# Performance work log

Measured on AMD Instinct MI355X. Metric: run time of the kernel, lower is better.

## Reference

```python
import jax, jax.numpy as jnp
import numpy as np

N = 100000        # points
C_IN = 64         # in_planes
C_OUT = 64        # out_planes (== mid_planes)
SHARE = 8         # share_planes
NS = 16           # nsample
CW = C_OUT // SHARE  # attention channels (8)
EPS = 1e-5


def _bn(x, gamma, beta):
    # PointBatchNorm in training mode: normalize over all axes except channel (last)
    ax = tuple(range(x.ndim - 1))
    m = jnp.mean(x, axis=ax)
    v = jnp.var(x, axis=ax)
    return gamma * (x - m) * jax.lax.rsqrt(v + EPS) + beta


def setup_inputs() -> dict:
    key = jax.random.key(0)
    ks = jax.random.split(key, 20)
    s = 0.05
    inp = {
        "p": jax.random.normal(ks[0], (N, 3), jnp.float32) * 5.0,
        "x": jax.random.normal(ks[1], (N, C_IN), jnp.float32),
        "o": jnp.array([N], jnp.int32),
        "idx": jax.random.randint(ks[2], (N, NS), 0, N, jnp.int32),
        # q/k/v linears
        "Wq": jax.random.normal(ks[3], (C_IN, C_OUT), jnp.float32) * s,
        "bq": jnp.zeros((C_OUT,), jnp.float32),
        "Wk": jax.random.normal(ks[4], (C_IN, C_OUT), jnp.float32) * s,
        "bk": jnp.zeros((C_OUT,), jnp.float32),
        "Wv": jax.random.normal(ks[5], (C_IN, C_OUT), jnp.float32) * s,
        "bv": jnp.zeros((C_OUT,), jnp.float32),
        # linear_p: Linear(3,3) -> BN(3) -> ReLU -> Linear(3,out)
        "Wp1": jax.random.normal(ks[6], (3, 3), jnp.float32) * 0.5,
        "bp1": jnp.zeros((3,), jnp.float32),
        "gp": jnp.ones((3,), jnp.float32),
        "betap": jnp.zeros((3,), jnp.float32),
        "Wp2": jax.random.normal(ks[7], (3, C_OUT), jnp.float32) * s,
        "bp2": jnp.zeros((C_OUT,), jnp.float32),
        # linear_w: BN(mid)->ReLU->Linear(mid, CW)->BN(CW)->ReLU->Linear(CW, CW)
        "gw1": jnp.ones((C_OUT,), jnp.float32),
        "bw1": jnp.zeros((C_OUT,), jnp.float32),
        "Ww1": jax.random.normal(ks[8], (C_OUT, CW), jnp.float32) * s,
        "bww1": jnp.zeros((CW,), jnp.float32),
        "gw2": jnp.ones((CW,), jnp.float32),
        "bw2": jnp.zeros((CW,), jnp.float32),
        "Ww2": jax.random.normal(ks[9], (CW, CW), jnp.float32) * s,
        "bww2": jnp.zeros((CW,), jnp.float32),
    }
    return inp


def reference(p, x, o, idx,
              Wq, bq, Wk, bk, Wv, bv,
              Wp1, bp1, gp, betap, Wp2, bp2,
              gw1, bw1, Ww1, bww1, gw2, bw2, Ww2, bww2):
    relu = jax.nn.relu
    x_q = x @ Wq + bq                       # [n, mid]
    x_k = x @ Wk + bk                       # [n, mid]
    x_v = x @ Wv + bv                       # [n, out]
    # knn_query_and_group: gather neighbors (idx precomputed), with relative xyz
    p_r0 = p[idx] - p[:, None, :]           # [n, ns, 3]
    xk_g = x_k[idx]                         # [n, ns, mid]
    xv_g = x_v[idx]                         # [n, ns, out]
    # linear_p
    p_r = relu(_bn(p_r0 @ Wp1 + bp1, gp, betap)) @ Wp2 + bp2   # [n, ns, out]
    # einops.reduce 'n ns (i j) -> n ns j' with j=mid_planes: i==1 -> identity
    r_qk = xk_g - x_q[:, None, :] + p_r     # [n, ns, mid]
    # linear_w
    w = relu(_bn(r_qk, gw1, bw1)) @ Ww1 + bww1          # [n, ns, CW]
    w = relu(_bn(w, gw2, bw2)) @ Ww2 + bww2             # [n, ns, CW]
    w = jax.nn.softmax(w, axis=1)                        # softmax over neighbors
    # shared-channel weighted sum
    v = (xv_g + p_r).reshape(N, NS, SHARE, CW)           # [n, ns, s, i]
    out = jnp.einsum('ntsi,nti->nsi', v, w)              # [n, s, i]
    return out.reshape(N, C_OUT)
```

## Files before the change

kernel.cpp:

```cpp
#include <hip/hip_runtime.h>
#include <math.h>

#define NPTS 100000
#define NSAMP 16
#define NROWS (NPTS*NSAMP)
#define EPS 1e-5f

#define NQKV ((NPTS + 63)/64)
#define GRID_B 1024
#define GRID_C 2048
#define GRID_D 2048
#define GRID_E 2048

#define S_BN1A 0
#define S_BN1B 4
#define S_BN2A 8
#define S_BN2B 72
#define S_BN3A 136
#define S_BN3B 144
#define S_PARTB 160
#define S_PARTC (S_PARTB + GRID_B*8)
#define S_PARTD (S_PARTC + GRID_C*128)

typedef __attribute__((ext_vector_type(8))) _Float16 f16x8;
typedef __attribute__((ext_vector_type(4))) float f32x4;

__device__ __forceinline__ float bf2f(unsigned short u) {
    return __uint_as_float(((unsigned int)u) << 16);
}
__device__ __forceinline__ unsigned int cvt_pk_bf16(float lo, float hi) {
    unsigned int r;
    asm("v_cvt_pk_bf16_f32 %0, %1, %2" : "=v"(r) : "v"(lo), "v"(hi));
    return r;
}
__device__ __forceinline__ float rlF(float v, int t) {
    return __int_as_float(__builtin_amdgcn_readlane(__float_as_int(v), t));
}

__global__ __launch_bounds__(256) void qkv_bn1_kernel(
    const float* __restrict__ x,
    const float* __restrict__ Wq, const float* __restrict__ bq,
    const float* __restrict__ Wk, const float* __restrict__ bk,
    const float* __restrict__ Wv, const float* __restrict__ bv,
    unsigned short* __restrict__ xqb, unsigned short* __restrict__ xkb,
    unsigned short* __restrict__ xvb,
    const float* __restrict__ p, const int* __restrict__ idx,
    const float* __restrict__ Wp1, const float* __restrict__ bp1,
    unsigned short* __restrict__ tb, float* __restrict__ part)
{
    __shared__ __align__(16) float xsh[64][68];
    __shared__ __align__(16) float wsh[64][64];
    __shared__ float red16[4][6];
    const int tid = threadIdx.x;

    if (blockIdx.x >= NQKV) {
        const int b = blockIdx.x - NQKV;
        float w9[9], bb[3];
        #pragma unroll
        for (int i = 0; i < 9; ++i) w9[i] = Wp1[i];
        #pragma unroll
        for (int i = 0; i < 3; ++i) bb[i] = bp1[i];

        float s0=0.f,s1=0.f,s2=0.f,q0=0.f,q1=0.f,q2=0.f;
        for (int row = b*256 + tid; row < NROWS; row += GRID_B*256) {
            const int n = row >> 4;
            const int j = idx[row];
            const float d0 = p[j*3+0] - p[n*3+0];
            const float d1 = p[j*3+1] - p[n*3+1];
            const float d2 = p[j*3+2] - p[n*3+2];
            const float t0 = d0*w9[0] + d1*w9[3] + d2*w9[6] + bb[0];
            const float t1 = d0*w9[1] + d1*w9[4] + d2*w9[7] + bb[1];
            const float t2 = d0*w9[2] + d1*w9[5] + d2*w9[8] + bb[2];
            uint2 o;
            o.x = cvt_pk_bf16(t0, t1);
            o.y = cvt_pk_bf16(t2, 0.f);
            *(uint2*)&tb[(size_t)row*4] = o;
            s0 += t0; s1 += t1; s2 += t2;
            q0 += t0*t0; q1 += t1*t1; q2 += t2*t2;
        }
        #pragma unroll
        for (int m = 32; m >= 1; m >>= 1) {
            s0 += __shfl_xor(s0, m); s1 += __shfl_xor(s1, m); s2 += __shfl_xor(s2, m);
            q0 += __shfl_xor(q0, m); q1 += __shfl_xor(q1, m); q2 += __shfl_xor(q2, m);
        }
        const int lane = tid & 63, wid = tid >> 6;
        if (lane == 0) {
            red16[wid][0]=s0; red16[wid][1]=s1; red16[wid][2]=s2;
            red16[wid][3]=q0; red16[wid][4]=q1; red16[wid][5]=q2;
        }
        __syncthreads();
        if (tid < 6)
            part[b*8 + tid] = red16[0][tid]+red16[1][tid]+red16[2][tid]+red16[3][tid];
        return;
    }

    const int r0 = blockIdx.x * 64;
    {
        const int row = tid >> 4, c4 = tid & 15;
        #pragma unroll
        for (int rr = 0; rr < 4; ++rr) {
            const int r = row + rr*16;
            const int gr = r0 + r;
            float4 v = (gr < NPTS) ? *(const float4*)&x[(size_t)gr*64 + c4*4]
                                   : make_float4(0.f, 0.f, 0.f, 0.f);
            *(float4*)&xsh[r][c4*4] = v;
        }
    }

    const int tr = tid >> 4, tc = tid & 15;

    for (int m = 0; m < 3; ++m) {
        const float* __restrict__ W  = (m == 0) ? Wq : (m == 1) ? Wk : Wv;
        const float* __restrict__ bs = (m == 0) ? bq : (m == 1) ? bk : bv;
        unsigned short* __restrict__ dst = (m == 0) ? xqb : (m == 1) ? xkb : xvb;

        __syncthreads();
        for (int l = tid; l < 1024; l += 256)
            *(float4*)&wsh[l >> 4][(l & 15)*4] = *(const float4*)&W[l*4];
        __syncthreads();

        float acc[4][4];
        {
            const float4 b4 = *(const float4*)&bs[tc*4];
            #pragma unroll
            for (int rr = 0; rr < 4; ++rr) {
                acc[rr][0] = b4.x; acc[rr][1] = b4.y;
                acc[rr][2] = b4.z; acc[rr][3] = b4.w;
            }
        }

        #pragma unroll 4
        for (int k4 = 0; k4 < 16; ++k4) {
            float4 xr[4];
            #pragma unroll
            for (int rr = 0; rr < 4; ++rr)
                xr[rr] = *(const float4*)&xsh[tr + 16*rr][k4*4];
            float4 wr[4];
            #pragma unroll
            for (int kk = 0; kk < 4; ++kk)
                wr[kk] = *(const float4*)&wsh[k4*4 + kk][tc*4];
            #pragma unroll
            for (int rr = 0; rr < 4; ++rr) {
                acc[rr][0] += xr[rr].x*wr[0].x + xr[rr].y*wr[1].x + xr[rr].z*wr[2].x + xr[rr].w*wr[3].x;
                acc[rr][1] += xr[rr].x*wr[0].y + xr[rr].y*wr[1].y + xr[rr].z*wr[2].y + xr[rr].w*wr[3].y;
                acc[rr][2] += xr[rr].x*wr[0].z + xr[rr].y*wr[1].z + xr[rr].z*wr[2].z + xr[rr].w*wr[3].z;
                acc[rr][3] += xr[rr].x*wr[0].w + xr[rr].y*wr[1].w + xr[rr].z*wr[2].w + xr[rr].w*wr[3].w;
            }
        }

        #pragma unroll
        for (int rr = 0; rr < 4; ++rr) {
            const int gr = r0 + tr + 16*rr;
            if (gr < NPTS) {
                uint2 o;
                o.x = cvt_pk_bf16(acc[rr][0], acc[rr][1]);
                o.y = cvt_pk_bf16(acc[rr][2], acc[rr][3]);
                *(uint2*)&dst[(size_t)gr*64 + tc*4] = o;
            }
        }
    }
}

__global__ __launch_bounds__(256) void bn_fin_kernel(
    const float* __restrict__ part, int nblk, int stride, int nch,
    const float* __restrict__ g, const float* __restrict__ beta,
    float* __restrict__ aout, float* __restrict__ bout)
{
    const int c = blockIdx.x;
    const int tid = threadIdx.x;
    float s = 0.f, q = 0.f;
    for (int b = tid; b < nblk; b += 256) {
        s += part[(size_t)b*stride + c];
        q += part[(size_t)b*stride + nch + c];
    }
    #pragma unroll
    for (int m = 32; m >= 1; m >>= 1) { s += __shfl_xor(s, m); q += __shfl_xor(q, m); }
    __shared__ float rs[4], rq[4];
    if ((tid & 63) == 0) { rs[tid >> 6] = s; rq[tid >> 6] = q; }
    __syncthreads();
    if (tid == 0) {
        s = rs[0]+rs[1]+rs[2]+rs[3];
        q = rq[0]+rq[1]+rq[2]+rq[3];
        const float inv = 1.0f / (float)NROWS;
        const float mean = s * inv;
        const float var = fmaxf(q * inv - mean*mean, 0.f);
        const float a = g[c] * rsqrtf(var + EPS);
        aout[c] = a;
        bout[c] = beta[c] - a * mean;
    }
}

__global__ __launch_bounds__(256, 8) void bn2_stats_kernel(
    const int* __restrict__ idx, const unsigned short* __restrict__ tb,
    const unsigned short* __restrict__ xqb, const unsigned short* __restrict__ xkb,
    const float* __restrict__ Wp2, const float* __restrict__ bp2,
    const float* __restrict__ st, float* __restrict__ part)
{
    const int tid = threadIdx.x, lane = tid & 63, wid = tid >> 6;
    float a1[3], b1[3];
    #pragma unroll
    for (int i = 0; i < 3; ++i) { a1[i] = st[S_BN1A+i]; b1[i] = st[S_BN1B+i]; }
    const float wc0 = Wp2[lane], wc1 = Wp2[64+lane], wc2 = Wp2[128+lane], bpc = bp2[lane];
    const int lane16 = lane & 15;

    float s = 0.f, q = 0.f;
    const int nw = gridDim.x * 4;
    for (int pt = blockIdx.x*4 + wid; pt < NPTS; pt += nw) {
        const float xqc = bf2f(xqb[(size_t)pt*64 + lane]);
        const int jreg = idx[pt*16 + lane16];
        const uint2 tv = *(const uint2*)&tb[(size_t)(pt*16 + lane16)*4];
        const float t0 = bf2f((unsigned short)tv.x);
        const float t1 = bf2f((unsigned short)(tv.x >> 16));
        const float t2 = bf2f((unsigned short)tv.y);
        const float h0 = fmaxf(a1[0]*t0 + b1[0], 0.f);
        const float h1 = fmaxf(a1[1]*t1 + b1[1], 0.f);
        const float h2 = fmaxf(a1[2]*t2 + b1[2], 0.f);

        #pragma unroll
        for (int t = 0; t < 16; ++t) {
            const int jt = __builtin_amdgcn_readlane(jreg, t);
            const float g0 = rlF(h0, t), g1 = rlF(h1, t), g2 = rlF(h2, t);
            const float pr = fmaf(g0, wc0, fmaf(g1, wc1, fmaf(g2, wc2, bpc)));
            const float r = bf2f(xkb[(size_t)jt*64 + lane]) - xqc + pr;
            s += r; q = fmaf(r, r, q);
        }
    }
    __shared__ float redS[4][64], redQ[4][64];
    redS[wid][lane] = s; redQ[wid][lane] = q;
    __syncthreads();
    if (tid < 64) {
        const float S = redS[0][tid]+redS[1][tid]+redS[2][tid]+redS[3][tid];
        const float Q = redQ[0][tid]+redQ[1][tid]+redQ[2][tid]+redQ[3][tid];
        part[(size_t)blockIdx.x*128 + tid] = S;
        part[(size_t)blockIdx.x*128 + 64 + tid] = Q;
    }
}

__global__ __launch_bounds__(256, 8) void w1_kernel(
    const int* __restrict__ idx, const unsigned short* __restrict__ tb,
    const unsigned short* __restrict__ xqb, const unsigned short* __restrict__ xkb,
    const float* __restrict__ Wp2, const float* __restrict__ bp2,
    const float* __restrict__ Ww1, const float* __restrict__ bww1,
    const float* __restrict__ st, unsigned short* __restrict__ w1out,
    float* __restrict__ part)
{
    __shared__ __align__(16) _Float16 hl[4][16][64];
    const int tid = threadIdx.x, lane = tid & 63, wid = tid >> 6;

    float a1[3], b1[3];
    #pragma unroll
    for (int i = 0; i < 3; ++i) { a1[i] = st[S_BN1A+i]; b1[i] = st[S_BN1B+i]; }

    const int c = lane;
    const float wc0 = Wp2[c], wc1 = Wp2[64+c], wc2 = Wp2[128+c], bpc = bp2[c];
    const float a2c = st[S_BN2A + c], b2c = st[S_BN2B + c];
    const int lane16 = lane & 15;
    const int kgrp = lane >> 4;

    f16x8 aF0, aF1;
    {
        const int m = lane16;
        #pragma unroll
        for (int i = 0; i < 8; ++i) {
            const int k0 = kgrp*4 + (i & 3) + 16*(i >> 2);
            const int i0 = (m < 8) ? (k0*8 + m) : 0;
            const int i1 = (m < 8) ? ((k0 + 32)*8 + m) : 0;
            aF0[i] = (m < 8) ? (_Float16)Ww1[i0] : (_Float16)0.f;
            aF1[i] = (m < 8) ? (_Float16)Ww1[i1] : (_Float16)0.f;
        }
    }
    f32x4 cb;
    #pragma unroll
    for (int r = 0; r < 4; ++r) cb[r] = bww1[(kgrp*4 + r) & 7];

    float s3[4] = {0.f,0.f,0.f,0.f}, q3[4] = {0.f,0.f,0.f,0.f};
    const int nw = gridDim.x * 4;
    for (int pt = blockIdx.x*4 + wid; pt < NPTS; pt += nw) {
        const float xqc = bf2f(xqb[(size_t)pt*64 + lane]);
        const int jreg = idx[pt*16 + lane16];
        const uint2 tv = *(const uint2*)&tb[(size_t)(pt*16 + lane16)*4];
        const float t0v = bf2f((unsigned short)tv.x);
        const float t1v = bf2f((unsigned short)(tv.x >> 16));
        const float t2v = bf2f((unsigned short)tv.y);
        const float h0 = fmaxf(a1[0]*t0v + b1[0], 0.f);
        const float h1 = fmaxf(a1[1]*t1v + b1[1], 0.f);
        const float h2 = fmaxf(a1[2]*t2v + b1[2], 0.f);

        #pragma unroll
        for (int t = 0; t < 16; ++t) {
            const int jt = __builtin_amdgcn_readlane(jreg, t);
            const float g0 = rlF(h0, t), g1 = rlF(h1, t), g2 = rlF(h2, t);
            const float pr = fmaf(g0, wc0, fmaf(g1, wc1, fmaf(g2, wc2, bpc)));
            const float r = bf2f(xkb[(size_t)jt*64 + lane]) - xqc + pr;
            hl[wid][t][lane ^ ((t & 7) << 3)] = (_Float16)fmaxf(fmaf(a2c, r, b2c), 0.f);
        }

        const int t = lane16;
        const int key = (t & 7) << 3;
        union { f16x8 v; uint2 u[2]; } b0u, b1u;
        b0u.u[0] = *(const uint2*)&hl[wid][t][(kgrp*4)      ^ key];
        b0u.u[1] = *(const uint2*)&hl[wid][t][(kgrp*4 + 16) ^ key];
        b1u.u[0] = *(const uint2*)&hl[wid][t][(kgrp*4 + 32) ^ key];
        b1u.u[1] = *(const uint2*)&hl[wid][t][(kgrp*4 + 48) ^ key];

        f32x4 acc = __builtin_amdgcn_mfma_f32_16x16x32_f16(aF0, b0u.v, cb, 0, 0, 0);
        acc = __builtin_amdgcn_mfma_f32_16x16x32_f16(aF1, b1u.v, acc, 0, 0, 0);

        if (lane < 32) {
            uint2 o;
            o.x = cvt_pk_bf16(acc[0], acc[1]);
            o.y = cvt_pk_bf16(acc[2], acc[3]);
            *(uint2*)&w1out[(size_t)pt*128 + lane16*8 + kgrp*4] = o;
            #pragma unroll
            for (int r = 0; r < 4; ++r) {
                s3[r] += acc[r];
                q3[r] = fmaf(acc[r], acc[r], q3[r]);
            }
        }
    }

    #pragma unroll
    for (int m = 8; m >= 1; m >>= 1) {
        #pragma unroll
        for (int r = 0; r < 4; ++r) {
            s3[r] += __shfl_xor(s3[r], m);
            q3[r] += __shfl_xor(q3[r], m);
        }
    }
    __shared__ float redS[4][8], redQ[4][8];
    if (lane == 0 || lane == 16) {
        const int jb = (lane >> 4) * 4;
        #pragma unroll
        for (int r = 0; r < 4; ++r) { redS[wid][jb+r] = s3[r]; redQ[wid][jb+r] = q3[r]; }
    }
    __syncthreads();
    if (tid < 8) {
        const float S = redS[0][tid]+redS[1][tid]+redS[2][tid]+redS[3][tid];
        const float Q = redQ[0][tid]+redQ[1][tid]+redQ[2][tid]+redQ[3][tid];
        part[(size_t)blockIdx.x*16 + tid]     = S;
        part[(size_t)blockIdx.x*16 + 8 + tid] = Q;
    }
}

__global__ __launch_bounds__(256, 8) void out_kernel(
    const int* __restrict__ idx, const unsigned short* __restrict__ tb,
    const unsigned short* __restrict__ xvb, const unsigned short* __restrict__ w1b,
    const float* __restrict__ Wp2, const float* __restrict__ bp2,
    const float* __restrict__ Ww2, const float* __restrict__ bww2,
    const float* __restrict__ st, float* __restrict__ out)
{
    __shared__ float wl[4][16][8];
    const int tid = threadIdx.x, lane = tid & 63, wid = tid >> 6;
    const int j8 = lane & 7, t0 = lane >> 3;
    const int lane16 = lane & 15;

    float a1[3], b1[3];
    #pragma unroll
    for (int i = 0; i < 3; ++i) { a1[i] = st[S_BN1A+i]; b1[i] = st[S_BN1B+i]; }
    float ww2c[8];
    #pragma unroll
    for (int i = 0; i < 8; ++i) ww2c[i] = Ww2[i*8 + j8];
    const float a3j = st[S_BN3A + j8], b3j = st[S_BN3B + j8];
    const float bw2j = bww2[j8];
    const int c = lane;
    const float wc0 = Wp2[c], wc1 = Wp2[64+c], wc2 = Wp2[128+c], bpc = bp2[c];

    const int nw = gridDim.x * 4;
    for (int pt = blockIdx.x*4 + wid; pt < NPTS; pt += nw) {
        const int jreg = idx[pt*16 + lane16];
        const uint2 tv = *(const uint2*)&tb[(size_t)(pt*16 + lane16)*4];
        const float t1v = bf2f((unsigned short)tv.x);
        const float t2v = bf2f((unsigned short)(tv.x >> 16));
        const float t3v = bf2f((unsigned short)tv.y);
        const float h0 = fmaxf(a1[0]*t1v + b1[0], 0.f);
        const float h1 = fmaxf(a1[1]*t2v + b1[1], 0.f);
        const float h2 = fmaxf(a1[2]*t3v + b1[2], 0.f);

        const float val0 = bf2f(w1b[(size_t)pt*128 + lane]);
        const float val1 = bf2f(w1b[(size_t)pt*128 + 64 + lane]);
        const float r0 = fmaxf(a3j*val0 + b3j, 0.f);
        const float r1 = fmaxf(a3j*val1 + b3j, 0.f);
        float v0 = bw2j, v1 = bw2j;
        const int gbase = lane & 56;
        #pragma unroll
        for (int jj = 0; jj < 8; ++jj) {
            v0 += __shfl(r0, gbase + jj) * ww2c[jj];
            v1 += __shfl(r1, gbase + jj) * ww2c[jj];
        }
        float e0 = __expf(v0), e1 = __expf(v1);
        float ssum = e0 + e1;
        ssum += __shfl_xor(ssum, 8);
        ssum += __shfl_xor(ssum, 16);
        ssum += __shfl_xor(ssum, 32);
        const float inv = 1.0f / ssum;
        wl[wid][t0][j8]     = e0 * inv;
        wl[wid][t0 + 8][j8] = e1 * inv;

        float acc = 0.f;
        #pragma unroll
        for (int t = 0; t < 16; ++t) {
            const int jt = __builtin_amdgcn_readlane(jreg, t);
            const float g0 = rlF(h0, t), g1 = rlF(h1, t), g2 = rlF(h2, t);
            const float pr = fmaf(g0, wc0, fmaf(g1, wc1, fmaf(g2, wc2, bpc)));
            const float wt = wl[wid][t][j8];
            acc = fmaf(bf2f(xvb[(size_t)jt*64 + c]) + pr, wt, acc);
        }
        out[(size_t)pt*64 + c] = acc;
    }
}

extern "C" void kernel_launch(void* const* d_in, const int* in_sizes, int n_in,
                              void* d_out, int out_size, void* d_ws, size_t ws_size,
                              hipStream_t stream)
{
    const float* p    = (const float*)d_in[0];
    const float* x    = (const float*)d_in[1];
    const int*   idx  = (const int*)d_in[3];
    const float* Wq   = (const float*)d_in[4];
    const float* bq   = (const float*)d_in[5];
    const float* Wk   = (const float*)d_in[6];
    const float* bk   = (const float*)d_in[7];
    const float* Wv   = (const float*)d_in[8];
    const float* bv   = (const float*)d_in[9];
    const float* Wp1  = (const float*)d_in[10];
    const float* bp1  = (const float*)d_in[11];
    const float* gp   = (const float*)d_in[12];
    const float* betap= (const float*)d_in[13];
    const float* Wp2  = (const float*)d_in[14];
    const float* bp2  = (const float*)d_in[15];
    const float* gw1  = (const float*)d_in[16];
    const float* bw1  = (const float*)d_in[17];
    const float* Ww1  = (const float*)d_in[18];
    const float* bww1 = (const float*)d_in[19];
    const float* gw2  = (const float*)d_in[20];
    const float* bw2  = (const float*)d_in[21];
    const float* Ww2  = (const float*)d_in[22];
    const float* bww2 = (const float*)d_in[23];

    float* out = (float*)d_out;
    float* ws  = (float*)d_ws;

    unsigned short* xqb = (unsigned short*)ws;
    unsigned short* xkb = (unsigned short*)(ws + (size_t)NPTS*32);
    unsigned short* xvb = (unsigned short*)(ws + (size_t)NPTS*64);
    unsigned short* w1b = (unsigned short*)(ws + (size_t)NPTS*96);
    unsigned short* tb  = (unsigned short*)(ws + (size_t)NPTS*160);
    float*          st  = ws + (size_t)NPTS*192;

    qkv_bn1_kernel<<<NQKV + GRID_B, 256, 0, stream>>>(
        x, Wq, bq, Wk, bk, Wv, bv, xqb, xkb, xvb,
        p, idx, Wp1, bp1, tb, st + S_PARTB);
    bn_fin_kernel<<<3, 256, 0, stream>>>(st + S_PARTB, GRID_B, 8, 3, gp, betap,
                                         st + S_BN1A, st + S_BN1B);

    bn2_stats_kernel<<<GRID_C, 256, 0, stream>>>(idx, tb, xqb, xkb, Wp2, bp2,
                                                 st, st + S_PARTC);
    bn_fin_kernel<<<64, 256, 0, stream>>>(st + S_PARTC, GRID_C, 128, 64, gw1, bw1,
                                          st + S_BN2A, st + S_BN2B);

    w1_kernel<<<GRID_D, 256, 0, stream>>>(idx, tb, xqb, xkb, Wp2, bp2,
                                          Ww1, bww1, st, w1b, st + S_PARTD);
    bn_fin_kernel<<<8, 256, 0, stream>>>(st + S_PARTD, GRID_D, 16, 8, gw2, bw2,
                                         st + S_BN3A, st + S_BN3B);

    out_kernel<<<GRID_E, 256, 0, stream>>>(idx, tb, xvb, w1b, Wp2, bp2,
                                           Ww2, bww2, st, out);
}
```

Before: 228.2 us.

## Precompute BN1+ReLU trunk once and read per-neighbor values via scalar loads

Adds a pass that applies the first BatchNorm affine and ReLU to the positional trunk buffer in place, so the three downstream kernels no longer recompute it. Those kernels now fetch idx and trunk values through wave-uniform (readfirstlane) pointers, which lets them use scalar loads in place of readlane broadcasts. The BN2 scale is also folded into the Wp2 weights and the bias term in w1_kernel. The cost is one extra kernel launch plus a read-write pass over the trunk buffer.

```diff
diff --git a/kernel.cpp b/kernel.cpp
--- a/kernel.cpp
+++ b/kernel.cpp
@@ -32,9 +32,6 @@
     unsigned int r;
     asm("v_cvt_pk_bf16_f32 %0, %1, %2" : "=v"(r) : "v"(lo), "v"(hi));
     return r;
-}
-__device__ __forceinline__ float rlF(float v, int t) {
-    return __int_as_float(__builtin_amdgcn_readlane(__float_as_int(v), t));
 }
 
 __global__ __launch_bounds__(256) void qkv_bn1_kernel(
@@ -190,38 +187,54 @@
     }
 }
 
+__global__ __launch_bounds__(256) void trunk_relu_kernel(
+    unsigned short* __restrict__ tb, const float* __restrict__ st)
+{
+    const float a0 = st[S_BN1A], a1 = st[S_BN1A+1], a2 = st[S_BN1A+2];
+    const float b0 = st[S_BN1B], b1 = st[S_BN1B+1], b2 = st[S_BN1B+2];
+    for (int row = blockIdx.x*256 + threadIdx.x; row < NROWS; row += gridDim.x*256) {
+        uint2 v = *(const uint2*)&tb[(size_t)row*4];
+        const float t0 = __uint_as_float(v.x << 16);
+        const float t1 = __uint_as_float(v.x & 0xffff0000u);
+        const float t2 = __uint_as_float(v.y << 16);
+        const float h0 = fmaxf(fmaf(a0, t0, b0), 0.f);
+        const float h1 = fmaxf(fmaf(a1, t1, b1), 0.f);
+        const float h2 = fmaxf(fmaf(a2, t2, b2), 0.f);
+        v.x = cvt_pk_bf16(h0, h1);
+        v.y = cvt_pk_bf16(h2, 0.f);
+        *(uint2*)&tb[(size_t)row*4] = v;
+    }
+}
+
 __global__ __launch_bounds__(256, 8) void bn2_stats_kernel(
-    const int* __restrict__ idx, const unsigned short* __restrict__ tb,
+    const int* __restrict__ idx, const unsigned short* __restrict__ hb,
     const unsigned short* __restrict__ xqb, const unsigned short* __restrict__ xkb,
     const float* __restrict__ Wp2, const float* __restrict__ bp2,
     const float* __restrict__ st, float* __restrict__ part)
 {
     const int tid = threadIdx.x, lane = tid & 63, wid = tid >> 6;
-    float a1[3], b1[3];
-    #pragma unroll
-    for (int i = 0; i < 3; ++i) { a1[i] = st[S_BN1A+i]; b1[i] = st[S_BN1B+i]; }
     const float wc0 = Wp2[lane], wc1 = Wp2[64+lane], wc2 = Wp2[128+lane], bpc = bp2[lane];
-    const int lane16 = lane & 15;
 
     float s = 0.f, q = 0.f;
     const int nw = gridDim.x * 4;
     for (int pt = blockIdx.x*4 + wid; pt < NPTS; pt += nw) {
-        const float xqc = bf2f(xqb[(size_t)pt*64 + lane]);
-        const int jreg = idx[pt*16 + lane16];
-        const uint2 tv = *(const uint2*)&tb[(size_t)(pt*16 + lane16)*4];
-        const float t0 = bf2f((unsigned short)tv.x);
-        const float t1 = bf2f((unsigned short)(tv.x >> 16));
-        const float t2 = bf2f((unsigned short)tv.y);
-        const float h0 = fmaxf(a1[0]*t0 + b1[0], 0.f);
-        const float h1 = fmaxf(a1[1]*t1 + b1[1], 0.f);
-        const float h2 = fmaxf(a1[2]*t2 + b1[2], 0.f);
+        const int pt_u = __builtin_amdgcn_readfirstlane(pt);
+        const float xqc = bf2f(xqb[(size_t)pt_u*64 + lane]);
+        const float base = bpc - xqc;
+        const int* __restrict__ irow = idx + (size_t)pt_u*16;
+        const unsigned short* __restrict__ hrow = hb + (size_t)pt_u*64;
 
         #pragma unroll
         for (int t = 0; t < 16; ++t) {
-            const int jt = __builtin_amdgcn_readlane(jreg, t);
-            const float g0 = rlF(h0, t), g1 = rlF(h1, t), g2 = rlF(h2, t);
-            const float pr = fmaf(g0, wc0, fmaf(g1, wc1, fmaf(g2, wc2, bpc)));
-            const float r = bf2f(xkb[(size_t)jt*64 + lane]) - xqc + pr;
+            const int jt = irow[t];
+            const uint2 hv = *(const uint2*)&hrow[t*4];
+            const float g0 = __uint_as_float(hv.x << 16);
+            const float g1 = __uint_as_float(hv.x & 0xffff0000u);
+            const float g2 = __uint_as_float(hv.y << 16);
+            float tmp = fmaf(g2, wc2, base);
+            tmp = fmaf(g1, wc1, tmp);
+            tmp = fmaf(g0, wc0, tmp);
+            const float r = bf2f(xkb[(size_t)jt*64 + lane]) + tmp;
             s += r; q = fmaf(r, r, q);
         }
     }
@@ -237,7 +250,7 @@
 }
 
 __global__ __launch_bounds__(256, 8) void w1_kernel(
-    const int* __restrict__ idx, const unsigned short* __restrict__ tb,
+    const int* __restrict__ idx, const unsigned short* __restrict__ hb,
     const unsigned short* __restrict__ xqb, const unsigned short* __restrict__ xkb,
     const float* __restrict__ Wp2, const float* __restrict__ bp2,
     const float* __restrict__ Ww1, const float* __restrict__ bww1,
@@ -247,13 +260,10 @@
     __shared__ __align__(16) _Float16 hl[4][16][64];
     const int tid = threadIdx.x, lane = tid & 63, wid = tid >> 6;
 
-    float a1[3], b1[3];
-    #pragma unroll
-    for (int i = 0; i < 3; ++i) { a1[i] = st[S_BN1A+i]; b1[i] = st[S_BN1B+i]; }
-
     const int c = lane;
-    const float wc0 = Wp2[c], wc1 = Wp2[64+c], wc2 = Wp2[128+c], bpc = bp2[c];
     const float a2c = st[S_BN2A + c], b2c = st[S_BN2B + c];
+    const float wc0 = a2c * Wp2[c], wc1 = a2c * Wp2[64+c], wc2 = a2c * Wp2[128+c];
+    const float bpc = bp2[c];
     const int lane16 = lane & 15;
     const int kgrp = lane >> 4;
 
@@ -276,23 +286,25 @@
     float s3[4] = {0.f,0.f,0.f,0.f}, q3[4] = {0.f,0.f,0.f,0.f};
     const int nw = gridDim.x * 4;
     for (int pt = blockIdx.x*4 + wid; pt < NPTS; pt += nw) {
-        const float xqc = bf2f(xqb[(size_t)pt*64 + lane]);
-        const int jreg = idx[pt*16 + lane16];
-        const uint2 tv = *(const uint2*)&tb[(size_t)(pt*16 + lane16)*4];
-        const float t0v = bf2f((unsigned short)tv.x);
-        const float t1v = bf2f((unsigned short)(tv.x >> 16));
-        const float t2v = bf2f((unsigned short)tv.y);
-        const float h0 = fmaxf(a1[0]*t0v + b1[0], 0.f);
-        const float h1 = fmaxf(a1[1]*t1v + b1[1], 0.f);
-        const float h2 = fmaxf(a1[2]*t2v + b1[2], 0.f);
+        const int pt_u = __builtin_amdgcn_readfirstlane(pt);
+        const float xqc = bf2f(xqb[(size_t)pt_u*64 + lane]);
+        const float base = fmaf(a2c, bpc - xqc, b2c);
+        const int* __restrict__ irow = idx + (size_t)pt_u*16;
+        const unsigned short* __restrict__ hrow = hb + (size_t)pt_u*64;
 
         #pragma unroll
         for (int t = 0; t < 16; ++t) {
-            const int jt = __builtin_amdgcn_readlane(jreg, t);
-            const float g0 = rlF(h0, t), g1 = rlF(h1, t), g2 = rlF(h2, t);
-            const float pr = fmaf(g0, wc0, fmaf(g1, wc1, fmaf(g2, wc2, bpc)));
-            const float r = bf2f(xkb[(size_t)jt*64 + lane]) - xqc + pr;
-            hl[wid][t][lane ^ ((t & 7) << 3)] = (_Float16)fmaxf(fmaf(a2c, r, b2c), 0.f);
+            const int jt = irow[t];
+            const uint2 hv = *(const uint2*)&hrow[t*4];
+            const float g0 = __uint_as_float(hv.x << 16);
+            const float g1 = __uint_as_float(hv.x & 0xffff0000u);
+            const float g2 = __uint_as_float(hv.y << 16);
+            float tmp = fmaf(g2, wc2, base);
+            tmp = fmaf(g1, wc1, tmp);
+            tmp = fmaf(g0, wc0, tmp);
+            const float xkval = bf2f(xkb[(size_t)jt*64 + lane]);
+            hl[wid][t][lane ^ ((t & 7) << 3)] =
+                (_Float16)fmaxf(fmaf(a2c, xkval, tmp), 0.f);
         }
 
         const int t = lane16;
@@ -343,7 +355,7 @@
 }
 
 __global__ __launch_bounds__(256, 8) void out_kernel(
-    const int* __restrict__ idx, const unsigned short* __restrict__ tb,
+    const int* __restrict__ idx, const unsigned short* __restrict__ hb,
     const unsigned short* __restrict__ xvb, const unsigned short* __restrict__ w1b,
     const float* __restrict__ Wp2, const float* __restrict__ bp2,
     const float* __restrict__ Ww2, const float* __restrict__ bww2,
@@ -352,11 +364,7 @@
     __shared__ float wl[4][16][8];
     const int tid = threadIdx.x, lane = tid & 63, wid = tid >> 6;
     const int j8 = lane & 7, t0 = lane >> 3;
-    const int lane16 = lane & 15;
-
-    float a1[3], b1[3];
-    #pragma unroll
-    for (int i = 0; i < 3; ++i) { a1[i] = st[S_BN1A+i]; b1[i] = st[S_BN1B+i]; }
+
     float ww2c[8];
     #pragma unroll
     for (int i = 0; i < 8; ++i) ww2c[i] = Ww2[i*8 + j8];
@@ -367,17 +375,12 @@
 
     const int nw = gridDim.x * 4;
     for (int pt = blockIdx.x*4 + wid; pt < NPTS; pt += nw) {
-        const int jreg = idx[pt*16 + lane16];
-        const uint2 tv = *(const uint2*)&tb[(size_t)(pt*16 + lane16)*4];
-        const float t1v = bf2f((unsigned short)tv.x);
-        const float t2v = bf2f((unsigned short)(tv.x >> 16));
-        const float t3v = bf2f((unsigned short)tv.y);
-        const float h0 = fmaxf(a1[0]*t1v + b1[0], 0.f);
-        const float h1 = fmaxf(a1[1]*t2v + b1[1], 0.f);
-        const float h2 = fmaxf(a1[2]*t3v + b1[2], 0.f);
-
-        const float val0 = bf2f(w1b[(size_t)pt*128 + lane]);
-        const float val1 = bf2f(w1b[(size_t)pt*128 + 64 + lane]);
+        const int pt_u = __builtin_amdgcn_readfirstlane(pt);
+        const int* __restrict__ irow = idx + (size_t)pt_u*16;
+        const unsigned short* __restrict__ hrow = hb + (size_t)pt_u*64;
+
+        const float val0 = bf2f(w1b[(size_t)pt_u*128 + lane]);
+        const float val1 = bf2f(w1b[(size_t)pt_u*128 + 64 + lane]);
         const float r0 = fmaxf(a3j*val0 + b3j, 0.f);
         const float r1 = fmaxf(a3j*val1 + b3j, 0.f);
         float v0 = bw2j, v1 = bw2j;
@@ -399,9 +402,14 @@
         float acc = 0.f;
         #pragma unroll
         for (int t = 0; t < 16; ++t) {
-            const int jt = __builtin_amdgcn_readlane(jreg, t);
-            const float g0 = rlF(h0, t), g1 = rlF(h1, t), g2 = rlF(h2, t);
-            const float pr = fmaf(g0, wc0, fmaf(g1, wc1, fmaf(g2, wc2, bpc)));
+            const int jt = irow[t];
+            const uint2 hv = *(const uint2*)&hrow[t*4];
+            const float g0 = __uint_as_float(hv.x << 16);
+            const float g1 = __uint_as_float(hv.x & 0xffff0000u);
+            const float g2 = __uint_as_float(hv.y << 16);
+            float pr = fmaf(g2, wc2, bpc);
+            pr = fmaf(g1, wc1, pr);
+            pr = fmaf(g0, wc0, pr);
             const float wt = wl[wid][t][j8];
             acc = fmaf(bf2f(xvb[(size_t)jt*64 + c]) + pr, wt, acc);
         }
@@ -452,6 +460,7 @@
         p, idx, Wp1, bp1, tb, st + S_PARTB);
     bn_fin_kernel<<<3, 256, 0, stream>>>(st + S_PARTB, GRID_B, 8, 3, gp, betap,
                                          st + S_BN1A, st + S_BN1B);
+    trunk_relu_kernel<<<1024, 256, 0, stream>>>(tb, st);
 
     bn2_stats_kernel<<<GRID_C, 256, 0, stream>>>(idx, tb, xqb, xkb, Wp2, bp2,
                                                  st, st + S_PARTC);
```

Result: slower. 246.3 us (+7.9%).
